# Kernel optimization log

Measured on AMD Instinct MI355X. Metric: run time of the kernel, lower is better.

Reference implementation:

```python
import jax, jax.numpy as jnp
import numpy as np

N_BINS = 229      # mel bins (H_dim == s_dim == N_BINS)
MODEL = 128       # model_complexity
OUT = 88          # output_features (piano keys)
W_SIZE = 30       # half-window; window length = 2*30+1 = 61
B, T = 4, 2048


def setup_inputs() -> dict:
    key = jax.random.key(0)
    ks = jax.random.split(key, 8)
    sF = 1.0 / np.sqrt(2 * N_BINS)   # attn linear fan_in = s_dim + H_dim
    sM = 1.0 / np.sqrt(MODEL)
    s1 = 1.0 / np.sqrt(N_BINS)
    return {
        "spec": jax.random.normal(ks[0], (B, T, N_BINS), jnp.float32),
        # attn = nn.Linear(s_dim + H_dim, model_size), split into hidden / encoder halves
        "W_h": jax.random.normal(ks[1], (N_BINS, MODEL), jnp.float32) * sF,
        "W_e": jax.random.normal(ks[2], (N_BINS, MODEL), jnp.float32) * sF,
        "b_attn": jax.random.normal(ks[3], (MODEL,), jnp.float32) * sF,
        # v = nn.Linear(model_size, 1, bias=False)
        "v_w": jax.random.normal(ks[4], (MODEL,), jnp.float32) * sM,
        # linear1 = nn.Linear(N_BINS, output_features) (layers=1, cat_feat=False)
        "W1": jax.random.normal(ks[5], (N_BINS, OUT), jnp.float32) * s1,
        "b1": jax.random.normal(ks[6], (OUT,), jnp.float32) * s1,
    }


def reference(spec, W_h, W_e, b_attn, v_w, W1, b1):
    # spec: [B, T, F]; both `x` (hidden) and `encoder_outputs` in the torch model.
    Bn, Tn, Fn = spec.shape
    Wlen = 2 * W_SIZE + 1
    # pad time axis and take sliding windows (as_strided equivalent)
    padded = jnp.pad(spec, ((0, 0), (W_SIZE, W_SIZE), (0, 0)))
    idx = jnp.arange(Tn)[:, None] + jnp.arange(Wlen)[None, :]          # [T, Wlen]
    windows = padded[:, idx]                                            # [B, T, Wlen, F]
    # attn(cat(hidden, enc)) = hidden @ W_h + enc @ W_e + b  (hidden identical over window)
    h_term = spec @ W_h + b_attn                                        # [B, T, M]
    e_term = jnp.einsum('btwf,fm->btwm', windows, W_e)                  # [B, T, Wlen, M]
    energy = jnp.tanh(h_term[:, :, None, :] + e_term)
    scores = energy @ v_w                                               # [B, T, Wlen]
    a = jax.nn.softmax(scores, axis=-1)
    weighted = jnp.einsum('btw,btwf->btf', a, windows)                  # [B, T, F]
    frame_pred = jax.nn.sigmoid(weighted @ W1 + b1)                     # [B, T, OUT]
    return frame_pred, a[:, :, None, :]                                 # a: [B, T, 1, Wlen]
```

## Files before the change

kernel.cpp:

```cpp
#include <hip/hip_runtime.h>
#include <math.h>

#define N_BINS 229
#define MODEL  128
#define OUTD   88
#define WSZ    30
#define WLEN   61
#define BB     4
#define TT     2048
#define CTANH  2.8853900817779268f

#define KPAD   256
#define NPAD   384
#define ROWS_F 8
#define FHALO  71
#define EPADU  68

typedef __attribute__((ext_vector_type(8))) short  short8v;
typedef __attribute__((ext_vector_type(4))) float  f32x4;

__device__ __forceinline__ unsigned short bf16_rne(float x) {
    unsigned int u = __float_as_uint(x);
    return (unsigned short)((u + 0x7FFFu + ((u >> 16) & 1u)) >> 16);
}
__device__ __forceinline__ float sigmoidf_(float x) {
    return __builtin_amdgcn_rcpf(1.0f + __expf(-x));
}

__global__ __launch_bounds__(256) void k_prep_w(
        const float* __restrict__ W_h, const float* __restrict__ W_e,
        const float* __restrict__ W1, unsigned short* __restrict__ Wt) {
    const int n = blockIdx.x;
    const int k = threadIdx.x;
    float v = 0.0f;
    if (k < N_BINS) {
        if (n < 128)      v = W_h[k * MODEL + n] * CTANH;
        else if (n < 256) v = W_e[k * MODEL + (n - 128)] * CTANH;
        else if (n < 344) v = W1[k * OUTD + (n - 256)];
    }
    Wt[n * KPAD + k] = bf16_rne(v);
}

__global__ __launch_bounds__(512, 4) void k_he_mfma(
        const float* __restrict__ spec,
        const unsigned short* __restrict__ Wt,
        const float* __restrict__ b_attn,
        float* __restrict__ H,
        unsigned int* __restrict__ Ebf,
        unsigned int* __restrict__ S1b) {
    const int tid   = threadIdx.x;
    const int lane  = tid & 63;
    const int wv    = tid >> 6;
    const int gm0   = blockIdx.x * 16;
    const int mfrag = lane & 15;
    const int kg    = lane >> 4;
    const int n0    = wv * 48;

    f32x4 acc0 = {0,0,0,0}, acc1 = {0,0,0,0}, acc2 = {0,0,0,0};

    const float* __restrict__ sp = spec + (size_t)(gm0 + mfrag) * N_BINS;
    const unsigned short* __restrict__ B0 = Wt + (size_t)(n0      + mfrag) * KPAD;
    const unsigned short* __restrict__ B1 = Wt + (size_t)(n0 + 16 + mfrag) * KPAD;
    const unsigned short* __restrict__ B2 = Wt + (size_t)(n0 + 32 + mfrag) * KPAD;

    for (int kb = 0; kb < 8; ++kb) {
        const int k0 = kb * 32 + kg * 8;
        float v[8];
#pragma unroll
        for (int j = 0; j < 8; ++j)
            v[j] = (k0 + j < N_BINS) ? sp[k0 + j] : 0.0f;
        short8v ah, al;
#pragma unroll
        for (int j = 0; j < 8; ++j) {
            const unsigned short h = bf16_rne(v[j]);
            const float rr = v[j] - __uint_as_float((unsigned int)h << 16);
            ah[j] = (short)h;
            al[j] = (short)bf16_rne(rr);
        }
        const short8v b0 = *(const short8v*)(B0 + k0);
        const short8v b1 = *(const short8v*)(B1 + k0);
        const short8v b2 = *(const short8v*)(B2 + k0);
        acc0 = __builtin_amdgcn_mfma_f32_16x16x32_bf16(ah, b0, acc0, 0, 0, 0);
        acc0 = __builtin_amdgcn_mfma_f32_16x16x32_bf16(al, b0, acc0, 0, 0, 0);
        acc1 = __builtin_amdgcn_mfma_f32_16x16x32_bf16(ah, b1, acc1, 0, 0, 0);
        acc1 = __builtin_amdgcn_mfma_f32_16x16x32_bf16(al, b1, acc1, 0, 0, 0);
        acc2 = __builtin_amdgcn_mfma_f32_16x16x32_bf16(ah, b2, acc2, 0, 0, 0);
        acc2 = __builtin_amdgcn_mfma_f32_16x16x32_bf16(al, b2, acc2, 0, 0, 0);
    }

#pragma unroll
    for (int t = 0; t < 3; ++t) {
        const f32x4 acc = (t == 0) ? acc0 : (t == 1) ? acc1 : acc2;
        const int gn = n0 + t * 16 + mfrag;
        if (gn < 128) {
            const float bc = b_attn[gn] * CTANH;
#pragma unroll
            for (int r = 0; r < 4; ++r) {
                const int gm = gm0 + (kg << 2) + r;
                H[(size_t)gm * MODEL + gn] = acc[r] + bc;
            }
        } else if (gn < 256) {
            const int ne = gn - 128;
#pragma unroll
            for (int r = 0; r < 4; ++r) {
                const float own = acc[r];
                const float pv  = __shfl_xor(own, 1, 64);
                if ((ne & 1) == 0) {
                    const int gm = gm0 + (kg << 2) + r;
                    Ebf[(size_t)gm * 64 + (ne >> 1)] =
                        (unsigned int)bf16_rne(own) |
                        ((unsigned int)bf16_rne(pv) << 16);
                }
            }
        } else if (gn < 344) {
            const int ns = gn - 256;
#pragma unroll
            for (int r = 0; r < 4; ++r) {
                const float own = acc[r];
                const float pv  = __shfl_xor(own, 1, 64);
                if ((ns & 1) == 0) {
                    const int gm = gm0 + (kg << 2) + r;
                    S1b[(size_t)gm * 44 + (ns >> 1)] =
                        (unsigned int)bf16_rne(own) |
                        ((unsigned int)bf16_rne(pv) << 16);
                }
            }
        }
    }
}

__global__ __launch_bounds__(512, 4) void k_fused(
        const float* __restrict__ H,
        const unsigned int* __restrict__ Ebf,
        const float* __restrict__ v_w,
        const unsigned int* __restrict__ S1b,
        const float* __restrict__ b1,
        float* __restrict__ pred,
        float* __restrict__ a_out) {
    const int nb   = blockIdx.x;
    const int tid  = threadIdx.x;
    const int wv   = tid >> 6;
    const int lane = tid & 63;
    const int r0   = nb * ROWS_F;
    const int b    = r0 >> 11;
    const int t0   = r0 & (TT - 1);
    const int r    = r0 + wv;
    const int t    = t0 + wv;

    __shared__ unsigned int Ebs[FHALO * EPADU];
    __shared__ unsigned int S1u[FHALO * 44];
    __shared__ float4 Hs4[ROWS_F * 32];
    __shared__ float4 Vs4[32];
    __shared__ float  scA[ROWS_F][64];

    const uint4* __restrict__ Eb16 = (const uint4*)Ebf + (size_t)b * TT * 16;
    for (int i = tid; i < FHALO * 16; i += 512) {
        const int row = i >> 4, c = i & 15;
        const int s   = t0 - WSZ + row;
        uint4 v = make_uint4(0u, 0u, 0u, 0u);
        if (s >= 0 && s < TT) v = Eb16[(size_t)s * 16 + c];
        *(uint4*)&Ebs[row * EPADU + (c << 2)] = v;
    }
    const uint4* __restrict__ Sb4 = (const uint4*)S1b + (size_t)b * TT * 11;
    for (int i = tid; i < FHALO * 11; i += 512) {
        const int row = i / 11, c = i - row * 11;
        const int s   = t0 - WSZ + row;
        uint4 v = make_uint4(0u, 0u, 0u, 0u);
        if (s >= 0 && s < TT) v = Sb4[(size_t)s * 11 + c];
        *(uint4*)&S1u[row * 44 + (c << 2)] = v;
    }
    if (tid < ROWS_F * 32)
        Hs4[tid] = ((const float4*)H)[(size_t)r0 * 32 + tid];
    else if (tid < ROWS_F * 32 + 32)
        Vs4[tid - ROWS_F * 32] = ((const float4*)v_w)[tid - ROWS_F * 32];
    __syncthreads();

    const int g  = lane & 3;
    const int w0 = lane >> 2;

    float vs = 0.f;
#pragma unroll
    for (int q = 0; q < 8; ++q) {
        const float4 vq = Vs4[(q << 2) + g];
        vs += (vq.x + vq.y) + (vq.z + vq.w);
    }
    vs += __shfl_xor(vs, 1, 64);
    vs += __shfl_xor(vs, 2, 64);

    int ro[4];
#pragma unroll
    for (int it = 0; it < 4; ++it)
        ro[it] = (wv + w0 + it * 16) * EPADU;

    const float4* __restrict__ HsR = &Hs4[wv * 32];

    float pp[4] = {0.f, 0.f, 0.f, 0.f};
#pragma unroll
    for (int q = 0; q < 8; ++q) {
        const int    cq = (q << 2) + g;
        const float4 hq = HsR[cq];
        const float4 vq = Vs4[cq];
        const float nx = -2.f * vq.x, ny = -2.f * vq.y,
                    nz = -2.f * vq.z, nw = -2.f * vq.w;
#pragma unroll
        for (int it = 0; it < 4; ++it) {
            const uint2 e2 = *(const uint2*)&Ebs[ro[it] + (cq << 1)];
            const float f0 = __uint_as_float(e2.x << 16);
            const float f1 = __uint_as_float(e2.x & 0xFFFF0000u);
            const float f2 = __uint_as_float(e2.y << 16);
            const float f3 = __uint_as_float(e2.y & 0xFFFF0000u);
            float u;
            u = __builtin_amdgcn_rcpf(__builtin_amdgcn_exp2f(f0 + hq.x) + 1.f);
            pp[it] = fmaf(nx, u, pp[it]);
            u = __builtin_amdgcn_rcpf(__builtin_amdgcn_exp2f(f1 + hq.y) + 1.f);
            pp[it] = fmaf(ny, u, pp[it]);
            u = __builtin_amdgcn_rcpf(__builtin_amdgcn_exp2f(f2 + hq.z) + 1.f);
            pp[it] = fmaf(nz, u, pp[it]);
            u = __builtin_amdgcn_rcpf(__builtin_amdgcn_exp2f(f3 + hq.w) + 1.f);
            pp[it] = fmaf(nw, u, pp[it]);
        }
    }
#pragma unroll
    for (int it = 0; it < 4; ++it) {
        float p = pp[it];
        p += __shfl_xor(p, 1, 64);
        p += __shfl_xor(p, 2, 64);
        const int w = w0 + it * 16;
        if (g == 0 && w < WLEN) scA[wv][w] = p + vs;
    }

    {
        float x = (lane < WLEN) ? scA[wv][lane] : -INFINITY;
        float mx = x;
#pragma unroll
        for (int d = 32; d >= 1; d >>= 1) mx = fmaxf(mx, __shfl_xor(mx, d, 64));
        float e = (lane < WLEN) ? __expf(x - mx) : 0.0f;
        float sm = e;
#pragma unroll
        for (int d = 32; d >= 1; d >>= 1) sm += __shfl_xor(sm, d, 64);
        const float a = e * __builtin_amdgcn_rcpf(sm);
        if (lane < WLEN) a_out[(size_t)r * WLEN + lane] = a;
        const int sl = t + lane - WSZ;
        scA[wv][lane] = (lane < WLEN && sl >= 0 && sl < TT) ? a : 0.0f;
    }

    if (lane < 44) {
        float a1 = 0.f, a2 = 0.f;
#pragma unroll 4
        for (int w = 0; w < 64; ++w) {
            const float at = scA[wv][w];
            const unsigned int pv = S1u[(wv + w) * 44 + lane];
            a1 = fmaf(at, __uint_as_float(pv << 16),         a1);
            a2 = fmaf(at, __uint_as_float(pv & 0xFFFF0000u), a2);
        }
        const int o = lane << 1;
        pred[(size_t)r * OUTD + o]     = sigmoidf_(a1 + b1[o]);
        pred[(size_t)r * OUTD + o + 1] = sigmoidf_(a2 + b1[o + 1]);
    }
}

extern "C" void kernel_launch(void* const* d_in, const int* in_sizes, int n_in,
                              void* d_out, int out_size, void* d_ws, size_t ws_size,
                              hipStream_t stream) {
    const float* spec   = (const float*)d_in[0];
    const float* W_h    = (const float*)d_in[1];
    const float* W_e    = (const float*)d_in[2];
    const float* b_attn = (const float*)d_in[3];
    const float* v_w    = (const float*)d_in[4];
    const float* W1     = (const float*)d_in[5];
    const float* b1     = (const float*)d_in[6];

    const int n_rows = BB * TT;
    char* ws = (char*)d_ws;
    float*          H   = (float*)ws;
    unsigned int*   Ebf = (unsigned int*)(ws + ((size_t)4 << 20));
    unsigned int*   S1b = (unsigned int*)(ws + ((size_t)6 << 20));
    unsigned short* Wt  = (unsigned short*)(ws + ((size_t)8 << 20));

    float* pred  = (float*)d_out;
    float* a_out = pred + (size_t)n_rows * OUTD;

    k_prep_w <<<NPAD,            256, 0, stream>>>(W_h, W_e, W1, Wt);
    k_he_mfma<<<n_rows / 16,     512, 0, stream>>>(spec, Wt, b_attn, H, Ebf, S1b);
    k_fused  <<<n_rows / ROWS_F, 512, 0, stream>>>(H, Ebf, v_w, S1b, b1,
                                                   pred, a_out);
}
```

Measured before the change: 56.08 us.

## Split projection GEMM across N-tiles per block and vectorize spec loads

The h/e/s1 projection kernel now launches three blocks per 16-row M tile, with each wave computing a single 16-wide N tile instead of three. This skips the padded tiles beyond 344 columns and raises parallelism. The K loop is unrolled, and its first seven iterations use unguarded 16-byte vector loads of spec, with only the tail kept bounds-checked. In exchange, each spec row is re-read and re-split into hi/lo bf16 by more waves, and some waves in the last part exit idle.

```diff
diff --git a/kernel.cpp b/kernel.cpp
--- a/kernel.cpp
+++ b/kernel.cpp
@@ -12,6 +12,7 @@
 
 #define KPAD   256
 #define NPAD   384
+#define NTILES 22
 #define ROWS_F 8
 #define FHALO  71
 #define EPADU  68
@@ -48,27 +49,28 @@
         float* __restrict__ H,
         unsigned int* __restrict__ Ebf,
         unsigned int* __restrict__ S1b) {
-    const int tid   = threadIdx.x;
-    const int lane  = tid & 63;
-    const int wv    = tid >> 6;
-    const int gm0   = blockIdx.x * 16;
+    const int tid  = threadIdx.x;
+    const int lane = tid & 63;
+    const int wv   = tid >> 6;
+    const int mt   = blockIdx.x / 3;
+    const int part = blockIdx.x - mt * 3;
+    const int tile = part * 8 + wv;
+    if (tile >= NTILES) return;
+    const int gm0   = mt * 16;
+    const int n0    = tile * 16;
     const int mfrag = lane & 15;
     const int kg    = lane >> 4;
-    const int n0    = wv * 48;
-
-    f32x4 acc0 = {0,0,0,0}, acc1 = {0,0,0,0}, acc2 = {0,0,0,0};
-
+
+    f32x4 acc = {0, 0, 0, 0};
     const float* __restrict__ sp = spec + (size_t)(gm0 + mfrag) * N_BINS;
-    const unsigned short* __restrict__ B0 = Wt + (size_t)(n0      + mfrag) * KPAD;
-    const unsigned short* __restrict__ B1 = Wt + (size_t)(n0 + 16 + mfrag) * KPAD;
-    const unsigned short* __restrict__ B2 = Wt + (size_t)(n0 + 32 + mfrag) * KPAD;
-
-    for (int kb = 0; kb < 8; ++kb) {
+    const unsigned short* __restrict__ Bp = Wt + (size_t)(n0 + mfrag) * KPAD;
+
+#pragma unroll
+    for (int kb = 0; kb < 7; ++kb) {
         const int k0 = kb * 32 + kg * 8;
         float v[8];
-#pragma unroll
-        for (int j = 0; j < 8; ++j)
-            v[j] = (k0 + j < N_BINS) ? sp[k0 + j] : 0.0f;
+        __builtin_memcpy(&v[0], sp + k0,     16);
+        __builtin_memcpy(&v[4], sp + k0 + 4, 16);
         short8v ah, al;
 #pragma unroll
         for (int j = 0; j < 8; ++j) {
@@ -77,53 +79,61 @@
             ah[j] = (short)h;
             al[j] = (short)bf16_rne(rr);
         }
-        const short8v b0 = *(const short8v*)(B0 + k0);
-        const short8v b1 = *(const short8v*)(B1 + k0);
-        const short8v b2 = *(const short8v*)(B2 + k0);
-        acc0 = __builtin_amdgcn_mfma_f32_16x16x32_bf16(ah, b0, acc0, 0, 0, 0);
-        acc0 = __builtin_amdgcn_mfma_f32_16x16x32_bf16(al, b0, acc0, 0, 0, 0);
-        acc1 = __builtin_amdgcn_mfma_f32_16x16x32_bf16(ah, b1, acc1, 0, 0, 0);
-        acc1 = __builtin_amdgcn_mfma_f32_16x16x32_bf16(al, b1, acc1, 0, 0, 0);
-        acc2 = __builtin_amdgcn_mfma_f32_16x16x32_bf16(ah, b2, acc2, 0, 0, 0);
-        acc2 = __builtin_amdgcn_mfma_f32_16x16x32_bf16(al, b2, acc2, 0, 0, 0);
-    }
-
-#pragma unroll
-    for (int t = 0; t < 3; ++t) {
-        const f32x4 acc = (t == 0) ? acc0 : (t == 1) ? acc1 : acc2;
-        const int gn = n0 + t * 16 + mfrag;
-        if (gn < 128) {
-            const float bc = b_attn[gn] * CTANH;
-#pragma unroll
-            for (int r = 0; r < 4; ++r) {
+        const short8v bb = *(const short8v*)(Bp + k0);
+        acc = __builtin_amdgcn_mfma_f32_16x16x32_bf16(ah, bb, acc, 0, 0, 0);
+        acc = __builtin_amdgcn_mfma_f32_16x16x32_bf16(al, bb, acc, 0, 0, 0);
+    }
+    {
+        const int k0 = 224 + kg * 8;
+        float v[8];
+#pragma unroll
+        for (int j = 0; j < 8; ++j)
+            v[j] = (k0 + j < N_BINS) ? sp[k0 + j] : 0.0f;
+        short8v ah, al;
+#pragma unroll
+        for (int j = 0; j < 8; ++j) {
+            const unsigned short h = bf16_rne(v[j]);
+            const float rr = v[j] - __uint_as_float((unsigned int)h << 16);
+            ah[j] = (short)h;
+            al[j] = (short)bf16_rne(rr);
+        }
+        const short8v bb = *(const short8v*)(Bp + k0);
+        acc = __builtin_amdgcn_mfma_f32_16x16x32_bf16(ah, bb, acc, 0, 0, 0);
+        acc = __builtin_amdgcn_mfma_f32_16x16x32_bf16(al, bb, acc, 0, 0, 0);
+    }
+
+    const int gn = n0 + mfrag;
+    if (gn < 128) {
+        const float bc = b_attn[gn] * CTANH;
+#pragma unroll
+        for (int r = 0; r < 4; ++r) {
+            const int gm = gm0 + (kg << 2) + r;
+            H[(size_t)gm * MODEL + gn] = acc[r] + bc;
+        }
+    } else if (gn < 256) {
+        const int ne = gn - 128;
+#pragma unroll
+        for (int r = 0; r < 4; ++r) {
+            const float own = acc[r];
+            const float pv  = __shfl_xor(own, 1, 64);
+            if ((ne & 1) == 0) {
                 const int gm = gm0 + (kg << 2) + r;
-                H[(size_t)gm * MODEL + gn] = acc[r] + bc;
+                Ebf[(size_t)gm * 64 + (ne >> 1)] =
+                    (unsigned int)bf16_rne(own) |
+                    ((unsigned int)bf16_rne(pv) << 16);
             }
-        } else if (gn < 256) {
-            const int ne = gn - 128;
-#pragma unroll
-            for (int r = 0; r < 4; ++r) {
-                const float own = acc[r];
-                const float pv  = __shfl_xor(own, 1, 64);
-                if ((ne & 1) == 0) {
-                    const int gm = gm0 + (kg << 2) + r;
-                    Ebf[(size_t)gm * 64 + (ne >> 1)] =
-                        (unsigned int)bf16_rne(own) |
-                        ((unsigned int)bf16_rne(pv) << 16);
-                }
-            }
-        } else if (gn < 344) {
-            const int ns = gn - 256;
-#pragma unroll
-            for (int r = 0; r < 4; ++r) {
-                const float own = acc[r];
-                const float pv  = __shfl_xor(own, 1, 64);
-                if ((ns & 1) == 0) {
-                    const int gm = gm0 + (kg << 2) + r;
-                    S1b[(size_t)gm * 44 + (ns >> 1)] =
-                        (unsigned int)bf16_rne(own) |
-                        ((unsigned int)bf16_rne(pv) << 16);
-                }
+        }
+    } else if (gn < 344) {
+        const int ns = gn - 256;
+#pragma unroll
+        for (int r = 0; r < 4; ++r) {
+            const float own = acc[r];
+            const float pv  = __shfl_xor(own, 1, 64);
+            if ((ns & 1) == 0) {
+                const int gm = gm0 + (kg << 2) + r;
+                S1b[(size_t)gm * 44 + (ns >> 1)] =
+                    (unsigned int)bf16_rne(own) |
+                    ((unsigned int)bf16_rne(pv) << 16);
             }
         }
     }
@@ -280,8 +290,8 @@
     float* pred  = (float*)d_out;
     float* a_out = pred + (size_t)n_rows * OUTD;
 
-    k_prep_w <<<NPAD,            256, 0, stream>>>(W_h, W_e, W1, Wt);
-    k_he_mfma<<<n_rows / 16,     512, 0, stream>>>(spec, Wt, b_attn, H, Ebf, S1b);
-    k_fused  <<<n_rows / ROWS_F, 512, 0, stream>>>(H, Ebf, v_w, S1b, b1,
-                                                   pred, a_out);
-}
+    k_prep_w <<<NPAD,              256, 0, stream>>>(W_h, W_e, W1, Wt);
+    k_he_mfma<<<(n_rows / 16) * 3, 512, 0, stream>>>(spec, Wt, b_attn, H, Ebf, S1b);
+    k_fused  <<<n_rows / ROWS_F,   512, 0, stream>>>(H, Ebf, v_w, S1b, b1,
+                                                     pred, a_out);
+}
```

After: 58.23 us. 3.8% more time.
